# Kernel tuning notes

Hardware: AMD Instinct MI355X
Metric: run time of the kernel (lower is better)

The kernel has to match this reference:

```python
import jax, jax.numpy as jnp
import numpy as np

N_NODES = 100_000
N_EDGES = 1_600_000
HID = 64
LAYERS = 3
MAX_ATOM = 100
BATCH = 16


def setup_inputs() -> dict:
    key = jax.random.key(0)
    ks = jax.random.split(key, 24)
    s = 0.05  # weight scale
    inp = {
        "x": jax.random.normal(ks[0], (N_NODES, 3), dtype=jnp.float32),
        "z": jax.random.randint(ks[1], (N_NODES,), 0, MAX_ATOM),
        "t": jax.random.uniform(ks[2], (BATCH, 1), dtype=jnp.float32),
        "edge_index": jax.random.randint(ks[3], (2, N_EDGES), 0, N_NODES),
        # atom embedding table
        "emb": jax.random.normal(ks[4], (MAX_ATOM, HID)) * s,
        # time embedding MLP: Linear(1,H), SiLU, Linear(H,H)
        "t_w1": jax.random.normal(ks[5], (1, HID)) * s,
        "t_b1": jnp.zeros((HID,)),
        "t_w2": jax.random.normal(ks[6], (HID, HID)) * s,
        "t_b2": jnp.zeros((HID,)),
        # per-layer EGNN params, stacked over layers
        # edge MLP: Linear(2H+1, H), SiLU, Linear(H, H), SiLU
        "e_w1": jax.random.normal(ks[7], (LAYERS, 2 * HID + 1, HID)) * s,
        "e_b1": jnp.zeros((LAYERS, HID)),
        "e_w2": jax.random.normal(ks[8], (LAYERS, HID, HID)) * s,
        "e_b2": jnp.zeros((LAYERS, HID)),
        # coord MLP: Linear(H, H), SiLU, Linear(H, 1)
        "c_w1": jax.random.normal(ks[9], (LAYERS, HID, HID)) * s,
        "c_b1": jnp.zeros((LAYERS, HID)),
        "c_w2": jax.random.normal(ks[10], (LAYERS, HID, 1)) * s,
        "c_b2": jnp.zeros((LAYERS, 1)),
        # node MLP: Linear(2H, H), SiLU, Linear(H, H), residual
        "n_w1": jax.random.normal(ks[11], (LAYERS, 2 * HID, HID)) * s,
        "n_b1": jnp.zeros((LAYERS, HID)),
        "n_w2": jax.random.normal(ks[12], (LAYERS, HID, HID)) * s,
        "n_b2": jnp.zeros((LAYERS, HID)),
    }
    return inp


def reference(x, z, t, edge_index, emb,
              t_w1, t_b1, t_w2, t_b2,
              e_w1, e_b1, e_w2, e_b2,
              c_w1, c_b1, c_w2, c_b2,
              n_w1, n_b1, n_w2, n_b2):
    silu = jax.nn.silu
    n = x.shape[0]
    # atom embedding + global time conditioning
    h = emb[z]                                           # (N, H)
    t_emb = silu(t @ t_w1 + t_b1) @ t_w2 + t_b2          # (B, H)
    h = h + jnp.mean(t_emb, axis=0, keepdims=True)
    src, dst = edge_index[0], edge_index[1]
    for l in range(LAYERS):
        diff = x[dst] - x[src]                           # (E, 3)
        d2 = jnp.sum(diff * diff, axis=-1, keepdims=True)  # (E, 1)
        ef = jnp.concatenate([h[dst], h[src], d2], axis=-1)  # (E, 2H+1)
        m = silu(silu(ef @ e_w1[l] + e_b1[l]) @ e_w2[l] + e_b2[l])  # (E, H)
        cw = silu(m @ c_w1[l] + c_b1[l]) @ c_w2[l] + c_b2[l]        # (E, 1)
        x = x + jax.ops.segment_sum(diff * cw, dst, num_segments=n)
        agg = jax.ops.segment_sum(m, dst, num_segments=n)           # (N, H)
        nf = jnp.concatenate([h, agg], axis=-1)                     # (N, 2H)
        h = h + (silu(nf @ n_w1[l] + n_b1[l]) @ n_w2[l] + n_b2[l])
    return x
```

## Files before the change

### kernel.cpp

```cpp
#include <hip/hip_runtime.h>

typedef __attribute__((ext_vector_type(8))) short s8v;
typedef __attribute__((ext_vector_type(4))) float f32x4;

#define MFMA16(A,B,C) __builtin_amdgcn_mfma_f32_16x16x32_bf16((A),(B),(C),0,0,0)

__device__ __forceinline__ float b2f(unsigned short s){
  union { unsigned u; float f; } v; v.u = ((unsigned)s) << 16; return v.f;
}
__device__ __forceinline__ unsigned short f2b(float f){
  union { float f; unsigned u; } v; v.f = f;
  return (unsigned short)((v.u + 0x8000u) >> 16);
}
__device__ __forceinline__ float siluf(float x){
  return x * __builtin_amdgcn_rcpf(1.f + __expf(-x));
}


__global__ void hist_kernel(const int* __restrict__ dst, int* __restrict__ deg, int E){
  int i = blockIdx.x*256 + threadIdx.x;
  if (i < E) atomicAdd(&deg[dst[i]], 1);
}

__global__ void scan1_kernel(const int* __restrict__ deg, int* __restrict__ rp,
                             int* __restrict__ bsum, int N){
  __shared__ int s[256];
  const int base = blockIdx.x*1024;
  const int t = threadIdx.x;
  int v[4];
  #pragma unroll
  for (int j = 0; j < 4; ++j){
    int idx = base + t*4 + j;
    int dv = (idx < N) ? deg[idx] : 0;
    v[j] = (dv + 3) & ~3;
  }
  const int tsum = v[0]+v[1]+v[2]+v[3];
  s[t] = tsum;
  __syncthreads();
  for (int off = 1; off < 256; off <<= 1){
    int x = (t >= off) ? s[t-off] : 0;
    __syncthreads();
    s[t] += x;
    __syncthreads();
  }
  const int incl = s[t];
  if (t == 255) bsum[blockIdx.x] = incl;
  int run = incl - tsum;
  #pragma unroll
  for (int j = 0; j < 4; ++j){
    int idx = base + t*4 + j;
    if (idx < N) rp[idx] = run;
    run += v[j];
  }
}

__global__ void scan2_kernel(int* __restrict__ bsum, int nb){
  __shared__ int s[256];
  const int t = threadIdx.x;
  const int v = (t < nb) ? bsum[t] : 0;
  s[t] = v;
  __syncthreads();
  for (int off = 1; off < 256; off <<= 1){
    int x = (t >= off) ? s[t-off] : 0;
    __syncthreads();
    s[t] += x;
    __syncthreads();
  }
  if (t < nb) bsum[t] = s[t] - v;
}

__global__ void scan3_kernel(int* __restrict__ rp, const int* __restrict__ bsum,
                             const int* __restrict__ deg, int N){
  int i = blockIdx.x*256 + threadIdx.x;
  if (i < N){
    int v = rp[i] + bsum[i >> 10];
    rp[i] = v;
    if (i == N-1) rp[N] = v + ((deg[i] + 3) & ~3);
  }
}

__global__ void scatter_slot_kernel(const int* __restrict__ src, const int* __restrict__ dst,
                                    const int* __restrict__ rp, int* __restrict__ cursor,
                                    int* __restrict__ csr_src, int* __restrict__ slot_meta,
                                    const int* __restrict__ deg, int E, int N){
  int i = blockIdx.x*256 + threadIdx.x;
  if (i < E){
    const int d = dst[i];
    const int pos = rp[d] + atomicAdd(&cursor[d], 1);
    csr_src[pos] = src[i];
  }
  if (i < N){
    const int base = rp[i];
    const int d = deg[i];
    const int ns = (d + 3) >> 2;
    const int s0 = base >> 2;
    for (int k = 0; k < ns; ++k){
      int c = d - k*4; c = (c > 4) ? 4 : c;
      slot_meta[s0 + k] = i | (c << 28);
    }
    for (int j = d; j < ns*4; ++j) csr_src[base + j] = i;
  }
  if (i == 0){
    const int S  = rp[N] >> 2;
    const int S4 = (S + 3) & ~3;
    for (int s = S; s < S4; ++s){
      slot_meta[s] = 0;
      for (int r = 0; r < 4; ++r) csr_src[s*4 + r] = 0;
    }
  }
}


__global__ void tmean_zero_kernel(const float* __restrict__ t,
                                  const float* __restrict__ tw1,
                                  const float* __restrict__ tb1,
                                  const float* __restrict__ tw2,
                                  const float* __restrict__ tb2,
                                  float* __restrict__ tmean,
                                  int* __restrict__ degcur, int n2){
  for (int k = blockIdx.x*256 + threadIdx.x; k < n2; k += gridDim.x*256)
    degcur[k] = 0;
  if (blockIdx.x == 0){
    __shared__ __align__(16) float s1[16*64];
    const int j = threadIdx.x & 63;
    const int grp = threadIdx.x >> 6;
    const float w1 = tw1[j], bb1 = tb1[j];
    #pragma unroll
    for (int b = grp*4; b < grp*4 + 4; ++b)
      s1[b*64 + j] = siluf(t[b] * w1 + bb1);
    __syncthreads();
    if (threadIdx.x < 64){
      float acc = 0.f;
      for (int b = 0; b < 16; ++b)
        for (int k = 0; k < 64; ++k)
          acc += s1[b*64 + k] * tw2[k*64 + j];
      tmean[j] = tb2[j] + acc * (1.f/16.f);
    }
  }
}

__global__ void init_h_kernel(const int* __restrict__ z,
                              const float* __restrict__ emb,
                              const float* __restrict__ tmean,
                              float* __restrict__ hf,
                              unsigned short* __restrict__ hb,
                              float* __restrict__ aggf, int N){
  int i = blockIdx.x*256 + threadIdx.x;
  if (i >= N*64) return;
  int j = i & 63;
  int n = i >> 6;
  float v = emb[z[n]*64 + j] + tmean[j];
  hf[i] = v;
  hb[i] = f2b(v);
  aggf[i] = 0.f;
}


__global__ __launch_bounds__(512) void p12_kernel(
    const unsigned short* __restrict__ hb,
    const float* __restrict__ ew1, const float* __restrict__ eb1,
    unsigned short* __restrict__ P1, unsigned short* __restrict__ P2,
    int layer, int N)
{
  __shared__ __align__(16) short w1a[64*72];
  __shared__ __align__(16) short w1b[64*72];
  __shared__ __align__(16) float b1s[64];

  const int tid = threadIdx.x;
  const float* w1g = ew1 + layer*129*64;
  for (int idx = tid; idx < 64*64; idx += 512){
    int k = idx >> 6, n = idx & 63;
    w1a[n*72 + k] = (short)f2b(w1g[k*64 + n]);
    w1b[n*72 + k] = (short)f2b(w1g[(64 + k)*64 + n]);
  }
  if (tid < 64) b1s[tid] = eb1[layer*64 + tid];
  __syncthreads();

  const int lane = tid & 63;
  const int wv = tid >> 6;
  const int q = lane >> 4;
  const int n16 = lane & 15;

  const int ntile = N >> 4;
  const int step = gridDim.x * 8;
  for (int t = blockIdx.x*8 + wv; t < ntile; t += step){
    const int row = t*16 + n16;
    const s8v* ph = (const s8v*)(hb + row*64);
    const s8v a0 = ph[q];
    const s8v a1 = ph[4+q];
    #pragma unroll
    for (int nt = 0; nt < 4; ++nt){
      const s8v* wa = (const s8v*)&w1a[(nt*16 + n16)*72];
      const s8v* wb = (const s8v*)&w1b[(nt*16 + n16)*72];
      f32x4 aA = {0.f,0.f,0.f,0.f};
      aA = MFMA16(a0, wa[q],   aA);
      aA = MFMA16(a1, wa[4+q], aA);
      f32x4 aB = {0.f,0.f,0.f,0.f};
      aB = MFMA16(a0, wb[q],   aB);
      aB = MFMA16(a1, wb[4+q], aB);
      const float bb = b1s[nt*16 + n16];
      #pragma unroll
      for (int r = 0; r < 4; ++r){
        const int o = (t*16 + q*4 + r)*64 + nt*16 + n16;
        P1[o] = f2b(aA[r] + bb);
        P2[o] = f2b(aB[r]);
      }
    }
  }
}


__global__ __launch_bounds__(512) void edge_tile_kernel(
    const int* __restrict__ rp, const int* __restrict__ csr_src,
    const int* __restrict__ slot_meta,
    const float* __restrict__ x_in, float* __restrict__ x_out,
    const unsigned short* __restrict__ P1, const unsigned short* __restrict__ P2,
    float* __restrict__ aggf,
    const float* __restrict__ ew1,
    const float* __restrict__ ew2, const float* __restrict__ eb2,
    const float* __restrict__ cw1, const float* __restrict__ cb1,
    const float* __restrict__ cw2, const float* __restrict__ cb2,
    int layer, int do_agg, int N)
{
  __shared__ __align__(16) short wT2[64*72];
  __shared__ __align__(16) short wc1T[64*72];
  __shared__ __align__(16) short sc[8][16*72];
  __shared__ __align__(16) float sdiff[8][48];

  const int tid = threadIdx.x;
  const float* w2g = ew2 + layer*64*64;
  const float* c1g = cw1 + layer*64*64;
  for (int idx = tid; idx < 64*64; idx += 512){
    int k = idx >> 6, n = idx & 63;
    wT2[n*72 + k]  = (short)f2b(w2g[k*64 + n]);
    wc1T[n*72 + k] = (short)f2b(c1g[k*64 + n]);
  }

  const int lane = tid & 63;
  const int wv = tid >> 6;
  const int q = lane >> 4;
  const int n16 = lane & 15;
  short* mysc = sc[wv];
  float* mydiff = sdiff[wv];

  const float* wlg = ew1 + layer*129*64 + 128*64;
  float wl_lo[8], wl_hi[8];
  #pragma unroll
  for (int j = 0; j < 8; ++j){
    wl_lo[j] = wlg[q*8 + j];
    wl_hi[j] = wlg[32 + q*8 + j];
  }
  float be2r[4], bc1r[4], cw2r[4];
  #pragma unroll
  for (int nt = 0; nt < 4; ++nt){
    be2r[nt] = eb2[layer*64 + nt*16 + n16];
    bc1r[nt] = cb1[layer*64 + nt*16 + n16];
    cw2r[nt] = cw2[layer*64 + nt*16 + n16];
  }
  const float cb2s = cb2[layer];
  __syncthreads();

  auto tile_compute = [&](int mo, float dx, float dy, float dz,
                          s8v lo1, s8v hi1, s8v lo2, s8v hi2, bool valid){
    const float d2 = dx*dx + dy*dy + dz*dz;
    if (q == 0){ mydiff[n16*3+0]=dx; mydiff[n16*3+1]=dy; mydiff[n16*3+2]=dz; }

    s8v alo, ahi;
    #pragma unroll
    for (int j = 0; j < 8; ++j){
      const float v0 = b2f((unsigned short)lo1[j]) + b2f((unsigned short)lo2[j]) + d2*wl_lo[j];
      alo[j] = (short)f2b(siluf(v0));
      const float v1 = b2f((unsigned short)hi1[j]) + b2f((unsigned short)hi2[j]) + d2*wl_hi[j];
      ahi[j] = (short)f2b(siluf(v1));
    }

    f32x4 acc2[4];
    #pragma unroll
    for (int nt = 0; nt < 4; ++nt){
      const s8v* wb = (const s8v*)&wT2[(nt*16 + n16)*72];
      f32x4 a = {0.f,0.f,0.f,0.f};
      a = MFMA16(alo, wb[q],   a);
      a = MFMA16(ahi, wb[4+q], a);
      acc2[nt] = a;
    }

    const int dn = mo & 0x0FFFFFFF;
    const int cnt = (int)(((unsigned)mo) >> 28);

    float colsum[4] = {0.f,0.f,0.f,0.f};
    #pragma unroll
    for (int nt = 0; nt < 4; ++nt){
      const float bb = be2r[nt];
      #pragma unroll
      for (int r = 0; r < 4; ++r){
        const float mv = siluf(acc2[nt][r] + bb);
        mysc[(q*4 + r)*72 + nt*16 + n16] = (short)f2b(mv);
        colsum[nt] += (r < cnt) ? mv : 0.f;
      }
    }
    __builtin_amdgcn_wave_barrier();
    const s8v* srd = (const s8v*)&mysc[n16*72];
    const s8v m0 = srd[q];
    const s8v m1 = srd[4+q];
    __builtin_amdgcn_wave_barrier();

    float pr[4] = {0.f,0.f,0.f,0.f};
    #pragma unroll
    for (int nt = 0; nt < 4; ++nt){
      const s8v* wb = (const s8v*)&wc1T[(nt*16 + n16)*72];
      f32x4 a = {0.f,0.f,0.f,0.f};
      a = MFMA16(m0, wb[q],   a);
      a = MFMA16(m1, wb[4+q], a);
      const float bc = bc1r[nt];
      const float wc2 = cw2r[nt];
      #pragma unroll
      for (int r = 0; r < 4; ++r) pr[r] += siluf(a[r] + bc) * wc2;
    }
    #pragma unroll
    for (int off = 1; off < 16; off <<= 1){
      #pragma unroll
      for (int r = 0; r < 4; ++r) pr[r] += __shfl_xor(pr[r], off, 64);
    }
    float xacc0 = 0.f, xacc1 = 0.f, xacc2 = 0.f;
    #pragma unroll
    for (int r = 0; r < 4; ++r){
      const float cwv = pr[r] + cb2s;
      xacc0 += mydiff[(q*4 + r)*3 + 0] * cwv;
      xacc1 += mydiff[(q*4 + r)*3 + 1] * cwv;
      xacc2 += mydiff[(q*4 + r)*3 + 2] * cwv;
    }

    const int dnb = __shfl_xor(dn, 16, 64);
    const bool same = (dnb == dn);
    #pragma unroll
    for (int nt = 0; nt < 4; ++nt){
      const float o = __shfl_xor(colsum[nt], 16, 64);
      if (same) colsum[nt] += o;
    }
    const float o0 = __shfl_xor(xacc0, 16, 64);
    const float o1 = __shfl_xor(xacc1, 16, 64);
    const float o2 = __shfl_xor(xacc2, 16, 64);
    if (same){ xacc0 += o0; xacc1 += o1; xacc2 += o2; }

    const bool writer = (((q & 1) == 0) || !same) && valid;
    if (do_agg && writer){
      #pragma unroll
      for (int nt = 0; nt < 4; ++nt)
        atomicAdd(&aggf[(size_t)dn*64 + nt*16 + n16], colsum[nt]);
    }
    if (writer && n16 < 3){
      const float v = (n16 == 0) ? xacc0 : (n16 == 1) ? xacc1 : xacc2;
      atomicAdd(&x_out[dn*3 + n16], v);
    }
  };

  const int T = (rp[N] + 15) >> 4;
  const int npair = (T + 1) >> 1;
  const int nwave = gridDim.x * 8;
  for (int pp = blockIdx.x*8 + wv; pp < npair; pp += nwave){
    const int ta = pp*2;
    const int tb = pp*2 + 1;
    const bool vb = (tb < T);
    const int tbb = vb ? tb : ta;

    const int miA = slot_meta[ta*4 + (n16 >> 2)];
    const int moA = slot_meta[ta*4 + q];
    const int siA = csr_src[ta*16 + n16];
    const int miB = slot_meta[tbb*4 + (n16 >> 2)];
    const int moB = slot_meta[tbb*4 + q];
    const int siB = csr_src[tbb*16 + n16];
    const int diA = miA & 0x0FFFFFFF;
    const int diB = miB & 0x0FFFFFFF;

    const float dxA = x_in[diA*3+0] - x_in[siA*3+0];
    const float dyA = x_in[diA*3+1] - x_in[siA*3+1];
    const float dzA = x_in[diA*3+2] - x_in[siA*3+2];
    const float dxB = x_in[diB*3+0] - x_in[siB*3+0];
    const float dyB = x_in[diB*3+1] - x_in[siB*3+1];
    const float dzB = x_in[diB*3+2] - x_in[siB*3+2];

    const s8v* pdA = (const s8v*)(P1 + (size_t)diA*64);
    const s8v lo1A = pdA[q], hi1A = pdA[4+q];
    const s8v* psA = (const s8v*)(P2 + (size_t)siA*64);
    const s8v lo2A = psA[q], hi2A = psA[4+q];
    const s8v* pdB = (const s8v*)(P1 + (size_t)diB*64);
    const s8v lo1B = pdB[q], hi1B = pdB[4+q];
    const s8v* psB = (const s8v*)(P2 + (size_t)siB*64);
    const s8v lo2B = psB[q], hi2B = psB[4+q];

    tile_compute(moA, dxA, dyA, dzA, lo1A, hi1A, lo2A, hi2A, true);
    tile_compute(moB, dxB, dyB, dzB, lo1B, hi1B, lo2B, hi2B, vb);
  }
}


__global__ __launch_bounds__(512) void node_p12_kernel(
    unsigned short* __restrict__ hb, float* __restrict__ hf,
    float* __restrict__ aggf,
    const float* __restrict__ nw1, const float* __restrict__ nb1,
    const float* __restrict__ nw2, const float* __restrict__ nb2,
    const float* __restrict__ ew1, const float* __restrict__ eb1,
    unsigned short* __restrict__ P1, unsigned short* __restrict__ P2,
    const float* __restrict__ xsrc, float* __restrict__ xdst,
    int layer, int do_zero, int N)
{
  __shared__ __align__(16) short wT1[64*136];
  __shared__ __align__(16) short wT2[64*72];
  __shared__ __align__(16) short w1a[64*72];
  __shared__ __align__(16) short w1b[64*72];
  __shared__ __align__(16) short sc[8][16*72];
  __shared__ __align__(16) float b1s[64];
  __shared__ __align__(16) float b2s[64];
  __shared__ __align__(16) float eb1s[64];

  const int tid = threadIdx.x;
  const float* w1g = nw1 + layer*128*64;
  const float* w2g = nw2 + layer*64*64;
  const float* e1g = ew1 + (layer+1)*129*64;
  for (int idx = tid; idx < 64*128; idx += 512){
    int k = idx >> 6, n = idx & 63;
    wT1[n*136 + k] = (short)f2b(w1g[k*64 + n]);
  }
  for (int idx = tid; idx < 64*64; idx += 512){
    int k = idx >> 6, n = idx & 63;
    wT2[n*72 + k] = (short)f2b(w2g[k*64 + n]);
    w1a[n*72 + k] = (short)f2b(e1g[k*64 + n]);
    w1b[n*72 + k] = (short)f2b(e1g[(64 + k)*64 + n]);
  }
  if (tid < 64){
    b1s[tid]  = nb1[layer*64 + tid];
    b2s[tid]  = nb2[layer*64 + tid];
    eb1s[tid] = eb1[(layer+1)*64 + tid];
  }
  __syncthreads();

  const int lane = tid & 63;
  const int wv = tid >> 6;
  const int q = lane >> 4;
  const int n16 = lane & 15;
  short* mysc = sc[wv];

  const int ntile = N >> 4;
  const int step = gridDim.x * 8;
  for (int t = blockIdx.x*8 + wv; t < ntile; t += step){
    const int row = t*16 + n16;
    const s8v* ph = (const s8v*)(hb + row*64);
    const s8v a0 = ph[q];
    const s8v a1 = ph[4+q];
    const f32x4* pa = (const f32x4*)(aggf + (size_t)row*64);
    const f32x4 u0 = pa[2*q];
    const f32x4 u1 = pa[2*q+1];
    const f32x4 u2 = pa[8+2*q];
    const f32x4 u3 = pa[9+2*q];
    s8v a2, a3;
    #pragma unroll
    for (int j = 0; j < 4; ++j){
      a2[j]   = (short)f2b(u0[j]);
      a2[4+j] = (short)f2b(u1[j]);
      a3[j]   = (short)f2b(u2[j]);
      a3[4+j] = (short)f2b(u3[j]);
    }
    if (do_zero){
      const f32x4 zz = {0.f,0.f,0.f,0.f};
      f32x4* pw = (f32x4*)(aggf + (size_t)row*64);
      pw[2*q] = zz; pw[2*q+1] = zz; pw[8+2*q] = zz; pw[9+2*q] = zz;
    }
    if (lane < 48) xdst[t*48 + lane] = xsrc[t*48 + lane];

    #pragma unroll
    for (int nt = 0; nt < 4; ++nt){
      const s8v* wb = (const s8v*)&wT1[(nt*16 + n16)*136];
      f32x4 a = {0.f,0.f,0.f,0.f};
      a = MFMA16(a0, wb[q],    a);
      a = MFMA16(a1, wb[4+q],  a);
      a = MFMA16(a2, wb[8+q],  a);
      a = MFMA16(a3, wb[12+q], a);
      const float bb = b1s[nt*16 + n16];
      #pragma unroll
      for (int r = 0; r < 4; ++r)
        mysc[(q*4 + r)*72 + nt*16 + n16] = (short)f2b(siluf(a[r] + bb));
    }
    __builtin_amdgcn_wave_barrier();
    const s8v* srd = (const s8v*)&mysc[n16*72];
    const s8v g0 = srd[q];
    const s8v g1 = srd[4+q];
    __builtin_amdgcn_wave_barrier();

    #pragma unroll
    for (int nt = 0; nt < 4; ++nt){
      const s8v* wb = (const s8v*)&wT2[(nt*16 + n16)*72];
      f32x4 a = {0.f,0.f,0.f,0.f};
      a = MFMA16(g0, wb[q],   a);
      a = MFMA16(g1, wb[4+q], a);
      const float bb = b2s[nt*16 + n16];
      #pragma unroll
      for (int r = 0; r < 4; ++r){
        const int idx = (t*16 + q*4 + r)*64 + nt*16 + n16;
        const float hv = hf[idx] + a[r] + bb;
        hf[idx] = hv;
        const unsigned short hvb = f2b(hv);
        hb[idx] = hvb;
        mysc[(q*4 + r)*72 + nt*16 + n16] = (short)hvb;
      }
    }
    __builtin_amdgcn_wave_barrier();
    const s8v h0 = srd[q];
    const s8v h1 = srd[4+q];
    __builtin_amdgcn_wave_barrier();

    #pragma unroll
    for (int nt = 0; nt < 4; ++nt){
      const s8v* wa = (const s8v*)&w1a[(nt*16 + n16)*72];
      const s8v* wb = (const s8v*)&w1b[(nt*16 + n16)*72];
      f32x4 aA = {0.f,0.f,0.f,0.f};
      aA = MFMA16(h0, wa[q],   aA);
      aA = MFMA16(h1, wa[4+q], aA);
      f32x4 aB = {0.f,0.f,0.f,0.f};
      aB = MFMA16(h0, wb[q],   aB);
      aB = MFMA16(h1, wb[4+q], aB);
      const float bb = eb1s[nt*16 + n16];
      #pragma unroll
      for (int r = 0; r < 4; ++r){
        const int o = (t*16 + q*4 + r)*64 + nt*16 + n16;
        P1[o] = f2b(aA[r] + bb);
        P2[o] = f2b(aB[r]);
      }
    }
  }
}


extern "C" void kernel_launch(void* const* d_in, const int* in_sizes, int n_in,
                              void* d_out, int out_size, void* d_ws, size_t ws_size,
                              hipStream_t stream)
{
  const float* x0   = (const float*)d_in[0];
  const int*   z    = (const int*)d_in[1];
  const float* tc   = (const float*)d_in[2];
  const int*   ei   = (const int*)d_in[3];
  const float* embc = (const float*)d_in[4];
  const float* tw1c = (const float*)d_in[5];
  const float* tb1c = (const float*)d_in[6];
  const float* tw2c = (const float*)d_in[7];
  const float* tb2c = (const float*)d_in[8];
  const float* ew1c = (const float*)d_in[9];
  const float* eb1c = (const float*)d_in[10];
  const float* ew2c = (const float*)d_in[11];
  const float* eb2c = (const float*)d_in[12];
  const float* cw1c = (const float*)d_in[13];
  const float* cb1c = (const float*)d_in[14];
  const float* cw2c = (const float*)d_in[15];
  const float* cb2c = (const float*)d_in[16];
  const float* nw1c = (const float*)d_in[17];
  const float* nb1c = (const float*)d_in[18];
  const float* nw2c = (const float*)d_in[19];
  const float* nb2c = (const float*)d_in[20];

  const int N = in_sizes[1];
  const int E = in_sizes[3] / 2;
  const int* srcp = ei;
  const int* dstp = ei + E;

  char* p = (char*)d_ws;
  auto alloc = [&](size_t bytes) -> void* {
    void* r = (void*)p; p += (bytes + 255) & ~(size_t)255; return r;
  };
  float* hf            = (float*)alloc((size_t)N*64*4);
  unsigned short* hbuf = (unsigned short*)alloc((size_t)N*64*2);
  float* aggf          = (float*)alloc((size_t)N*64*4);
  unsigned short* P1   = (unsigned short*)alloc((size_t)N*64*2);
  unsigned short* P2   = (unsigned short*)alloc((size_t)N*64*2);
  float* xa            = (float*)alloc((size_t)N*3*4);
  float* xb            = (float*)alloc((size_t)N*3*4);
  float* tmean         = (float*)alloc(64*4);
  int*   degcur        = (int*)alloc((size_t)2*N*4);
  int*   deg           = degcur;
  int*   cursor        = degcur + N;
  int*   rowp          = (int*)alloc((size_t)(N+1)*4);
  int*   bsum          = (int*)alloc(256*4);
  int*   csr_src       = (int*)alloc(((size_t)E + 3*(size_t)N + 64)*4);
  int*   slot_meta     = (int*)alloc(((size_t)E/4 + (size_t)N + 16)*4);

  tmean_zero_kernel<<<512, 256, 0, stream>>>(tc, tw1c, tb1c, tw2c, tb2c,
                                             tmean, degcur, 2*N);
  init_h_kernel<<<(N*64 + 255)/256, 256, 0, stream>>>(z, embc, tmean, hf, hbuf, aggf, N);

  hist_kernel<<<(E + 255)/256, 256, 0, stream>>>(dstp, deg, E);
  const int nb = (N + 1023)/1024;
  scan1_kernel<<<nb, 256, 0, stream>>>(deg, rowp, bsum, N);
  scan2_kernel<<<1, 256, 0, stream>>>(bsum, nb);
  scan3_kernel<<<(N + 255)/256, 256, 0, stream>>>(rowp, bsum, deg, N);
  scatter_slot_kernel<<<(E + 255)/256, 256, 0, stream>>>(srcp, dstp, rowp, cursor,
                                                         csr_src, slot_meta, deg, E, N);

  p12_kernel<<<512, 512, 0, stream>>>(hbuf, ew1c, eb1c, P1, P2, 0, N);

  const float* xc = x0;
  float* xnexts[3] = {xa, xb, (float*)d_out};
  (void)hipMemcpyAsync(xa, x0, (size_t)N*3*4, hipMemcpyDeviceToDevice, stream);
  for (int l = 0; l < 3; ++l){
    float* xout = xnexts[l];
    edge_tile_kernel<<<1024, 512, 0, stream>>>(rowp, csr_src, slot_meta, xc, xout,
        P1, P2, aggf,
        ew1c, ew2c, eb2c, cw1c, cb1c, cw2c, cb2c, l, (l < 2) ? 1 : 0, N);
    if (l < 2)
      node_p12_kernel<<<512, 512, 0, stream>>>(hbuf, hf, aggf,
          nw1c, nb1c, nw2c, nb2c, ew1c, eb1c, P1, P2,
          xout, xnexts[l+1], l, (l == 0) ? 1 : 0, N);
    xc = xout;
  }
}
```

Baseline: 775.4 us.

## Merge scan kernels, fold x copy into init, pack bf16 converts, skip dead h writes

```diff
diff --git a/kernel.cpp b/kernel.cpp
--- a/kernel.cpp
+++ b/kernel.cpp
@@ -11,6 +11,11 @@
 __device__ __forceinline__ unsigned short f2b(float f){
   union { float f; unsigned u; } v; v.f = f;
   return (unsigned short)((v.u + 0x8000u) >> 16);
+}
+__device__ __forceinline__ unsigned cvtpk(float lo, float hi){
+  unsigned r;
+  asm("v_cvt_pk_bf16_f32 %0, %1, %2" : "=v"(r) : "v"(lo), "v"(hi));
+  return r;
 }
 __device__ __forceinline__ float siluf(float x){
   return x * __builtin_amdgcn_rcpf(1.f + __expf(-x));
@@ -54,28 +59,26 @@
   }
 }
 
-__global__ void scan2_kernel(int* __restrict__ bsum, int nb){
-  __shared__ int s[256];
+__global__ void scan3_kernel(int* __restrict__ rp, const int* __restrict__ bsum,
+                             const int* __restrict__ deg, int N, int nb){
+  __shared__ int sb[256];
+  __shared__ int so[256];
   const int t = threadIdx.x;
   const int v = (t < nb) ? bsum[t] : 0;
-  s[t] = v;
+  sb[t] = v; so[t] = v;
   __syncthreads();
   for (int off = 1; off < 256; off <<= 1){
-    int x = (t >= off) ? s[t-off] : 0;
+    int x = (t >= off) ? sb[t-off] : 0;
     __syncthreads();
-    s[t] += x;
+    sb[t] += x;
     __syncthreads();
   }
-  if (t < nb) bsum[t] = s[t] - v;
-}
-
-__global__ void scan3_kernel(int* __restrict__ rp, const int* __restrict__ bsum,
-                             const int* __restrict__ deg, int N){
-  int i = blockIdx.x*256 + threadIdx.x;
+  int i = blockIdx.x*256 + t;
   if (i < N){
-    int v = rp[i] + bsum[i >> 10];
-    rp[i] = v;
-    if (i == N-1) rp[N] = v + ((deg[i] + 3) & ~3);
+    const int k = i >> 10;
+    const int val = rp[i] + (sb[k] - so[k]);
+    rp[i] = val;
+    if (i == N-1) rp[N] = val + ((deg[i] + 3) & ~3);
   }
 }
 
@@ -144,8 +147,11 @@
                               const float* __restrict__ tmean,
                               float* __restrict__ hf,
                               unsigned short* __restrict__ hb,
-                              float* __restrict__ aggf, int N){
+                              float* __restrict__ aggf,
+                              const float* __restrict__ x0,
+                              float* __restrict__ xa, int N){
   int i = blockIdx.x*256 + threadIdx.x;
+  if (i < N*3) xa[i] = x0[i];
   if (i >= N*64) return;
   int j = i & 63;
   int n = i >> 6;
@@ -263,15 +269,22 @@
   auto tile_compute = [&](int mo, float dx, float dy, float dz,
                           s8v lo1, s8v hi1, s8v lo2, s8v hi2, bool valid){
     const float d2 = dx*dx + dy*dy + dz*dz;
-    if (q == 0){ mydiff[n16*3+0]=dx; mydiff[n16*3+1]=dy; mydiff[n16*3+2]=dz; }
+    if (q == 0){ mydiff[n16] = dx; mydiff[16+n16] = dy; mydiff[32+n16] = dz; }
 
     s8v alo, ahi;
-    #pragma unroll
-    for (int j = 0; j < 8; ++j){
-      const float v0 = b2f((unsigned short)lo1[j]) + b2f((unsigned short)lo2[j]) + d2*wl_lo[j];
-      alo[j] = (short)f2b(siluf(v0));
-      const float v1 = b2f((unsigned short)hi1[j]) + b2f((unsigned short)hi2[j]) + d2*wl_hi[j];
-      ahi[j] = (short)f2b(siluf(v1));
+    {
+      union { unsigned u[4]; s8v s; } ua, ub;
+      #pragma unroll
+      for (int jp = 0; jp < 4; ++jp){
+        const int j0 = 2*jp, j1 = 2*jp + 1;
+        const float a0f = siluf(b2f((unsigned short)lo1[j0]) + b2f((unsigned short)lo2[j0]) + d2*wl_lo[j0]);
+        const float a1f = siluf(b2f((unsigned short)lo1[j1]) + b2f((unsigned short)lo2[j1]) + d2*wl_lo[j1]);
+        ua.u[jp] = cvtpk(a0f, a1f);
+        const float b0f = siluf(b2f((unsigned short)hi1[j0]) + b2f((unsigned short)hi2[j0]) + d2*wl_hi[j0]);
+        const float b1f = siluf(b2f((unsigned short)hi1[j1]) + b2f((unsigned short)hi2[j1]) + d2*wl_hi[j1]);
+        ub.u[jp] = cvtpk(b0f, b1f);
+      }
+      alo = ua.s; ahi = ub.s;
     }
 
     f32x4 acc2[4];
@@ -321,13 +334,16 @@
       #pragma unroll
       for (int r = 0; r < 4; ++r) pr[r] += __shfl_xor(pr[r], off, 64);
     }
+    const f32x4 dfx = *(const f32x4*)&mydiff[q*4];
+    const f32x4 dfy = *(const f32x4*)&mydiff[16 + q*4];
+    const f32x4 dfz = *(const f32x4*)&mydiff[32 + q*4];
     float xacc0 = 0.f, xacc1 = 0.f, xacc2 = 0.f;
     #pragma unroll
     for (int r = 0; r < 4; ++r){
       const float cwv = pr[r] + cb2s;
-      xacc0 += mydiff[(q*4 + r)*3 + 0] * cwv;
-      xacc1 += mydiff[(q*4 + r)*3 + 1] * cwv;
-      xacc2 += mydiff[(q*4 + r)*3 + 2] * cwv;
+      xacc0 += dfx[r] * cwv;
+      xacc1 += dfy[r] * cwv;
+      xacc2 += dfz[r] * cwv;
     }
 
     const int dnb = __shfl_xor(dn, 16, 64);
@@ -402,7 +418,7 @@
     const float* __restrict__ ew1, const float* __restrict__ eb1,
     unsigned short* __restrict__ P1, unsigned short* __restrict__ P2,
     const float* __restrict__ xsrc, float* __restrict__ xdst,
-    int layer, int do_zero, int N)
+    int layer, int do_zero, int do_h, int N)
 {
   __shared__ __align__(16) short wT1[64*136];
   __shared__ __align__(16) short wT2[64*72];
@@ -497,9 +513,8 @@
       for (int r = 0; r < 4; ++r){
         const int idx = (t*16 + q*4 + r)*64 + nt*16 + n16;
         const float hv = hf[idx] + a[r] + bb;
-        hf[idx] = hv;
         const unsigned short hvb = f2b(hv);
-        hb[idx] = hvb;
+        if (do_h){ hf[idx] = hv; hb[idx] = hvb; }
         mysc[(q*4 + r)*72 + nt*16 + n16] = (short)hvb;
       }
     }
@@ -583,13 +598,13 @@
 
   tmean_zero_kernel<<<512, 256, 0, stream>>>(tc, tw1c, tb1c, tw2c, tb2c,
                                              tmean, degcur, 2*N);
-  init_h_kernel<<<(N*64 + 255)/256, 256, 0, stream>>>(z, embc, tmean, hf, hbuf, aggf, N);
+  init_h_kernel<<<(N*64 + 255)/256, 256, 0, stream>>>(z, embc, tmean, hf, hbuf,
+                                                      aggf, x0, xa, N);
 
   hist_kernel<<<(E + 255)/256, 256, 0, stream>>>(dstp, deg, E);
   const int nb = (N + 1023)/1024;
   scan1_kernel<<<nb, 256, 0, stream>>>(deg, rowp, bsum, N);
-  scan2_kernel<<<1, 256, 0, stream>>>(bsum, nb);
-  scan3_kernel<<<(N + 255)/256, 256, 0, stream>>>(rowp, bsum, deg, N);
+  scan3_kernel<<<(N + 255)/256, 256, 0, stream>>>(rowp, bsum, deg, N, nb);
   scatter_slot_kernel<<<(E + 255)/256, 256, 0, stream>>>(srcp, dstp, rowp, cursor,
                                                          csr_src, slot_meta, deg, E, N);
 
@@ -597,7 +612,6 @@
 
   const float* xc = x0;
   float* xnexts[3] = {xa, xb, (float*)d_out};
-  (void)hipMemcpyAsync(xa, x0, (size_t)N*3*4, hipMemcpyDeviceToDevice, stream);
   for (int l = 0; l < 3; ++l){
     float* xout = xnexts[l];
     edge_tile_kernel<<<1024, 512, 0, stream>>>(rowp, csr_src, slot_meta, xc, xout,
@@ -606,7 +620,7 @@
     if (l < 2)
       node_p12_kernel<<<512, 512, 0, stream>>>(hbuf, hf, aggf,
           nw1c, nb1c, nw2c, nb2c, ew1c, eb1c, P1, P2,
-          xout, xnexts[l+1], l, (l == 0) ? 1 : 0, N);
+          xout, xnexts[l+1], l, (l == 0) ? 1 : 0, (l == 0) ? 1 : 0, N);
     xc = xout;
   }
 }
```

New measurement: 770.0 us. Within noise of the previous version (-0.7%).
